# Kernel optimization log

Hardware: AMD Instinct MI355X
Metric: run time of the kernel (lower is better)

## Reference

```python
import jax, jax.numpy as jnp
import numpy as np

VOCAB, D, H, HK, DH, M, DFF, NCLS = 32000, 512, 8, 2, 64, 64, 2048, 2
G = H // HK  # GQA group size = 4
EPS = 1e-6


def rmsnorm(x, g):
    return x * jax.lax.rsqrt(jnp.mean(x * x, axis=-1, keepdims=True) + EPS) * g


def setup_inputs() -> dict:
    key = jax.random.key(0)
    ks = jax.random.split(key, 14)
    s = 0.02
    return {
        "input_ids": jax.random.randint(ks[0], (8, 8192), 0, VOCAB),
        "emb": jax.random.normal(ks[1], (VOCAB, D), jnp.float32) * s,
        "Wq": jax.random.normal(ks[2], (D, H * DH), jnp.float32) * s,
        "Wk": jax.random.normal(ks[3], (D, HK * DH), jnp.float32) * s,
        "Wv": jax.random.normal(ks[4], (D, HK * DH), jnp.float32) * s,
        "Wphi": jax.random.normal(ks[5], (DH, M), jnp.float32),  # Laplacian kernel feature projection
        "Wo": jax.random.normal(ks[6], (H * DH, D), jnp.float32) * s,
        "g1": jnp.ones((D,), jnp.float32),
        "g2": jnp.ones((D,), jnp.float32),
        "Wg": jax.random.normal(ks[7], (D, DFF), jnp.float32) * s,
        "Wu": jax.random.normal(ks[8], (D, DFF), jnp.float32) * s,  # frozen up_proj (freeze only affects training, not math)
        "Wd": jax.random.normal(ks[9], (DFF, D), jnp.float32) * s,
        "Wc": jax.random.normal(ks[10], (D, NCLS), jnp.float32) * s,
        "bc": jnp.zeros((NCLS,), jnp.float32),
    }


def reference(input_ids, emb, Wq, Wk, Wv, Wphi, Wo, g1, g2, Wg, Wu, Wd, Wc, bc):
    B, S = input_ids.shape
    x = emb[input_ids]  # [B,S,D] embedding gather
    # --- kernelized (Laplacian) bidirectional GQA linear attention, pre-norm ---
    h = rmsnorm(x, g1)
    q = (h @ Wq).reshape(B, S, H, DH)
    k = (h @ Wk).reshape(B, S, HK, DH)
    v = (h @ Wv).reshape(B, S, HK, DH)
    # Laplacian positive feature map: phi(u) = exp(-|u @ Wphi|)  -> [.., M]
    pq = jnp.exp(-jnp.abs(jnp.einsum("bshd,dm->bshm", q, Wphi)))
    pk = jnp.exp(-jnp.abs(jnp.einsum("bskd,dm->bskm", k, Wphi)))
    # global (bidirectional) state per kv head: [B,HK,M,DH] and normalizer [B,HK,M]
    kv = jnp.einsum("bskm,bskd->bkmd", pk, v)
    z = pk.sum(axis=1)
    pqg = pq.reshape(B, S, HK, G, M)  # group query heads onto kv heads
    num = jnp.einsum("bskgm,bkmd->bskgd", pqg, kv)
    den = jnp.einsum("bskgm,bkm->bskg", pqg, z)
    attn = (num / (den[..., None] + EPS)).reshape(B, S, H * DH)
    x = x + attn @ Wo
    # --- SwiGLU FFN, pre-norm ---
    h2 = rmsnorm(x, g2)
    x = x + (jax.nn.silu(h2 @ Wg) * (h2 @ Wu)) @ Wd
    # --- mean pool + linear head ---
    logits = x.mean(axis=1) @ Wc + bc  # [B, NCLS]
    return logits
```

## Files before the change

kernel.cpp:

```cpp
#include <hip/hip_runtime.h>
#include <hip/hip_bf16.h>
#include <math.h>

typedef __attribute__((ext_vector_type(8))) short bf16x8;
typedef __attribute__((ext_vector_type(4))) float f32x4;

#define DEV static __device__ __forceinline__
#define AS1 __attribute__((address_space(1)))
#define AS3 __attribute__((address_space(3)))

DEV float bf2f(__hip_bfloat16 v) { return __bfloat162float(v); }
DEV __hip_bfloat16 f2bf(float f) { return __float2bfloat16(f); }
DEV float us2f(unsigned short u) { return __uint_as_float(((unsigned int)u) << 16); }
DEV unsigned short f2us(float f) {
    __hip_bfloat16 b = __float2bfloat16(f);
    return *(unsigned short*)&b;
}

DEV void gload_lds16(const void* g, void* l) {
    __builtin_amdgcn_global_load_lds((const AS1 unsigned int*)g,
                                     (AS3 unsigned int*)l, 16, 0, 0);
}

DEV void load8(const void* p, size_t off, int f32m, float* o) {
    if (f32m) {
        const float4* r = (const float4*)((const float*)p + off);
        float4 A = r[0], B = r[1];
        o[0] = A.x; o[1] = A.y; o[2] = A.z; o[3] = A.w;
        o[4] = B.x; o[5] = B.y; o[6] = B.z; o[7] = B.w;
    } else {
        const ushort4* r = (const ushort4*)((const __hip_bfloat16*)p + off);
        ushort4 A = r[0], B = r[1];
        o[0] = us2f(A.x); o[1] = us2f(A.y); o[2] = us2f(A.z); o[3] = us2f(A.w);
        o[4] = us2f(B.x); o[5] = us2f(B.y); o[6] = us2f(B.z); o[7] = us2f(B.w);
    }
}

DEV float loadElem(const void* p, size_t idx, int f32m) {
    return f32m ? ((const float*)p)[idx] : bf2f(((const __hip_bfloat16*)p)[idx]);
}

constexpr int NTOK = 65536;

constexpr size_t OFF_WQPT = 0;
constexpr size_t OFF_WKPT = OFF_WQPT + 524288ull;
constexpr size_t OFF_WVT  = OFF_WKPT + 131072ull;
constexpr size_t OFF_WOT  = OFF_WVT  + 131072ull;
constexpr size_t OFF_WGT  = OFF_WOT  + 524288ull;
constexpr size_t OFF_WUT  = OFF_WGT  + 2097152ull;
constexpr size_t OFF_KV   = OFF_WUT  + 2097152ull;
constexpr size_t OFF_Z    = OFF_KV   + 262144ull;
constexpr size_t OFF_POOL = OFF_Z    + 4096ull;
constexpr size_t OFF_TSUM = OFF_POOL + 16384ull;
constexpr size_t OFF_FLAG = OFF_TSUM + 65536ull;
constexpr size_t PERSIST  = OFF_FLAG + 256ull;
constexpr size_t OFF_H    = PERSIST;
constexpr size_t CHUNKBASE = OFF_H + 67108864ull;
constexpr int    ZERO_FLOATS = (262144 + 4096 + 16384 + 65536) / 4;
constexpr size_t PERTOK = 3584ull;

__global__ __launch_bounds__(128) void detect_kernel(
    const unsigned int* __restrict__ w, int* __restrict__ flag)
{
    __shared__ int cnt;
    if (threadIdx.x == 0) cnt = 0;
    __syncthreads();
    unsigned int v = w[threadIdx.x];
    float a = fabsf(us2f((unsigned short)(v & 0xFFFFu)));
    if (a >= 0.0625f && a <= 8.0f) atomicAdd(&cnt, 1);
    __syncthreads();
    if (threadIdx.x == 0) *flag = (cnt < 64) ? 1 : 0;
}

__global__ __launch_bounds__(256) void zero_kernel(float* __restrict__ p, int n)
{
    int i = blockIdx.x * 256 + threadIdx.x;
    if (i < n) p[i] = 0.0f;
}

__global__ __launch_bounds__(256) void fuse_phi_kernel(
    const void* __restrict__ W, const void* __restrict__ Wphi,
    __hip_bfloat16* __restrict__ outT, int wld, const int* __restrict__ flag)
{
    const int f = *flag;
    int o = blockIdx.x * 256 + threadIdx.x;
    int hm = o >> 9, d = o & 511;
    int h = hm >> 6, m = hm & 63;
    float acc = 0.f;
    if (f) {
        const float* Wf = (const float*)W;
        const float* Pf = (const float*)Wphi;
        #pragma unroll 8
        for (int dh = 0; dh < 64; ++dh)
            acc += Wf[(size_t)d * wld + h * 64 + dh] * Pf[dh * 64 + m];
    } else {
        const __hip_bfloat16* Wb = (const __hip_bfloat16*)W;
        const __hip_bfloat16* Pb = (const __hip_bfloat16*)Wphi;
        #pragma unroll 8
        for (int dh = 0; dh < 64; ++dh)
            acc += bf2f(Wb[(size_t)d * wld + h * 64 + dh]) * bf2f(Pb[dh * 64 + m]);
    }
    outT[o] = f2bf(acc);
}

__global__ __launch_bounds__(256) void transpose_kernel(
    const void* __restrict__ src, __hip_bfloat16* __restrict__ dst, int R, int Ccols,
    const int* __restrict__ flag)
{
    __shared__ float tile[32][33];
    const int f = *flag;
    const int tx = threadIdx.x & 31, ty = threadIdx.x >> 5;
    const int c0 = blockIdx.x * 32, r0 = blockIdx.y * 32;
    #pragma unroll
    for (int k = 0; k < 4; ++k) {
        const int rl = ty + k * 8;
        tile[rl][tx] = loadElem(src, (size_t)(r0 + rl) * Ccols + c0 + tx, f);
    }
    __syncthreads();
    #pragma unroll
    for (int k = 0; k < 4; ++k) {
        const int cl = ty + k * 8;
        dst[(size_t)(c0 + cl) * R + r0 + tx] = f2bf(tile[tx][cl]);
    }
}

__global__ __launch_bounds__(256) void embed_rms_kernel(
    const int* __restrict__ ids, const void* __restrict__ emb,
    const void* __restrict__ g1, __hip_bfloat16* __restrict__ h,
    const int* __restrict__ flag)
{
    const int f = *flag;
    const int n = blockIdx.x * 4 + (threadIdx.x >> 6);
    const int lane = threadIdx.x & 63;
    const int id = ids[n];
    float x[8];
    load8(emb, (size_t)id * 512 + lane * 8, f, x);
    float ss = 0.f;
    #pragma unroll
    for (int i = 0; i < 8; ++i) ss += x[i] * x[i];
    #pragma unroll
    for (int off = 32; off; off >>= 1) ss += __shfl_xor(ss, off, 64);
    const float scale = rsqrtf(ss * (1.0f / 512.0f) + 1e-6f);
    float gv[8];
    load8(g1, (size_t)lane * 8, f, gv);
    ushort4 h0, h1;
    h0.x = f2us(x[0] * scale * gv[0]); h0.y = f2us(x[1] * scale * gv[1]);
    h0.z = f2us(x[2] * scale * gv[2]); h0.w = f2us(x[3] * scale * gv[3]);
    h1.x = f2us(x[4] * scale * gv[4]); h1.y = f2us(x[5] * scale * gv[5]);
    h1.z = f2us(x[6] * scale * gv[6]); h1.w = f2us(x[7] * scale * gv[7]);
    ushort4* ho = (ushort4*)(h + (size_t)n * 512 + lane * 8);
    ho[0] = h0; ho[1] = h1;
}

__global__ __launch_bounds__(256) void rms2_kernel(
    const float* __restrict__ xf, const void* __restrict__ g2,
    __hip_bfloat16* __restrict__ h, const int* __restrict__ flag)
{
    const int f = *flag;
    const int n = blockIdx.x * 4 + (threadIdx.x >> 6);
    const int lane = threadIdx.x & 63;
    const float4* xr = (const float4*)(xf + (size_t)n * 512);
    float4 a = xr[lane * 2], b = xr[lane * 2 + 1];
    float x[8] = { a.x, a.y, a.z, a.w, b.x, b.y, b.z, b.w };
    float ss = 0.f;
    #pragma unroll
    for (int i = 0; i < 8; ++i) ss += x[i] * x[i];
    #pragma unroll
    for (int off = 32; off; off >>= 1) ss += __shfl_xor(ss, off, 64);
    const float scale = rsqrtf(ss * (1.0f / 512.0f) + 1e-6f);
    float gv[8];
    load8(g2, (size_t)lane * 8, f, gv);
    ushort4 h0, h1;
    h0.x = f2us(x[0] * scale * gv[0]); h0.y = f2us(x[1] * scale * gv[1]);
    h0.z = f2us(x[2] * scale * gv[2]); h0.w = f2us(x[3] * scale * gv[3]);
    h1.x = f2us(x[4] * scale * gv[4]); h1.y = f2us(x[5] * scale * gv[5]);
    h1.z = f2us(x[6] * scale * gv[6]); h1.w = f2us(x[7] * scale * gv[7]);
    ushort4* ho = (ushort4*)(h + (size_t)n * 512 + lane * 8);
    ho[0] = h0; ho[1] = h1;
}

template<int MODE>
__global__ __launch_bounds__(256) void gemm128_kernel(
    const __hip_bfloat16* __restrict__ A, const __hip_bfloat16* __restrict__ Bt,
    float* __restrict__ xf, __hip_bfloat16* __restrict__ Cout2,
    float* __restrict__ pooled, const int* __restrict__ ids,
    const void* __restrict__ emb, const int* __restrict__ flag, int gbase, int K)
{
    __shared__ __align__(16) char As[8192];
    __shared__ __align__(16) char Bs[8192];
    __shared__ int idsL[128];

    const int tid = threadIdx.x;
    const int bm = blockIdx.x, bn = blockIdx.y;
    const int wave = tid >> 6, lane = tid & 63;
    const int quad = lane >> 4, lr = lane & 15;
    const int wm = (wave >> 1) << 6, wn = (wave & 1) << 6;

    if (MODE == 7 && tid < 128) idsL[tid] = ids[bm * 128 + tid];

    const int srow = (wave << 5) + (lane >> 2);
    const int scol = lane & 3;
    const int sfr  = (srow + (srow >> 2)) & 3;
    const int sofs = ((scol ^ sfr) << 3);

    const __hip_bfloat16* ga0 = A  + (size_t)(bm * 128 + srow) * K + sofs;
    const __hip_bfloat16* gb0 = Bt + (size_t)(bn * 128 + srow) * K + sofs;
    const __hip_bfloat16* ga1 = ga0 + (size_t)16 * K;
    const __hip_bfloat16* gb1 = gb0 + (size_t)16 * K;
    char* lA0 = As + (wave << 11);
    char* lA1 = lA0 + 1024;
    char* lB0 = Bs + (wave << 11);
    char* lB1 = lB0 + 1024;

    const int fl  = (lr + (lr >> 2)) & 3;
    const int ac  = (quad ^ fl) << 4;
    const char* arp = As + ((wm + lr) << 6) + ac;
    const char* brp = Bs + ((wn + lr) << 6) + ac;

    f32x4 acc[4][4];
    #pragma unroll
    for (int i = 0; i < 4; ++i)
        #pragma unroll
        for (int j = 0; j < 4; ++j)
            #pragma unroll
            for (int r = 0; r < 4; ++r) acc[i][j][r] = 0.0f;

    for (int k0 = 0; k0 < K; k0 += 32) {
        __syncthreads();
        gload_lds16(ga0 + k0, lA0);
        gload_lds16(ga1 + k0, lA1);
        gload_lds16(gb0 + k0, lB0);
        gload_lds16(gb1 + k0, lB1);
        __syncthreads();

        bf16x8 af[4], bfr[4];
        #pragma unroll
        for (int i = 0; i < 4; ++i)
            af[i] = *(const bf16x8*)(arp + i * 1024);
        #pragma unroll
        for (int j = 0; j < 4; ++j)
            bfr[j] = *(const bf16x8*)(brp + j * 1024);
        #pragma unroll
        for (int i = 0; i < 4; ++i)
            #pragma unroll
            for (int j = 0; j < 4; ++j)
                acc[i][j] = __builtin_amdgcn_mfma_f32_16x16x32_bf16(af[i], bfr[j], acc[i][j], 0, 0, 0);
    }

    const int col0 = bn * 128 + wn + lr;

    if (MODE == 7) {
        const int f = *flag;
        const int b = (gbase + bm * 128) >> 13;
        #pragma unroll
        for (int j = 0; j < 4; ++j) {
            const int col = col0 + j * 16;
            float s = 0.f;
            #pragma unroll
            for (int i = 0; i < 4; ++i)
                #pragma unroll
                for (int r = 0; r < 4; ++r) {
                    const int rl = wm + i * 16 + quad * 4 + r;
                    const float e = loadElem(emb, (size_t)idsL[rl] * 512 + col, f);
                    const float w = e + acc[i][j][r];
                    xf[(size_t)(bm * 128 + rl) * 512 + col] = w;
                    s += w;
                }
            s += __shfl_xor(s, 16, 64);
            s += __shfl_xor(s, 32, 64);
            if (quad == 0) atomicAdd(&pooled[b * 512 + col], s);
        }
        return;
    }

    const int row0 = bm * 128 + wm + quad * 4;
    #pragma unroll
    for (int i = 0; i < 4; ++i)
        #pragma unroll
        for (int j = 0; j < 4; ++j) {
            const int col = col0 + j * 16;
            #pragma unroll
            for (int r = 0; r < 4; ++r) {
                const int row = row0 + i * 16 + r;
                const float v = acc[i][j][r];
                Cout2[(size_t)row * 256 + col] = f2bf(bn == 0 ? expf(-fabsf(v)) : v);
            }
        }
}

__global__ __launch_bounds__(256, 2) void pq_mix_kernel(
    const __hip_bfloat16* __restrict__ h, const __hip_bfloat16* __restrict__ WQPt,
    const float* __restrict__ kvf, const float* __restrict__ zf,
    __hip_bfloat16* __restrict__ attn, int gbase, int K)
{
    __shared__ __align__(16) char As[8192];
    __shared__ __align__(16) char Bs[8192];
    __shared__ __align__(16) char Pl[128 * 272];
    __shared__ __align__(16) __hip_bfloat16 kvT[80][72];

    const int tid = threadIdx.x;
    const int bm = blockIdx.x, bn = blockIdx.y;
    const int kh = bn >> 1;
    const int wave = tid >> 6, lane = tid & 63;
    const int quad = lane >> 4, lr = lane & 15;
    const int wm = (wave >> 1) << 6, wn = (wave & 1) << 6;
    const int b = (gbase + bm * 128) >> 13;

    {
        const float* kvsrc = kvf + ((size_t)b * 2 + kh) * 4096;
        for (int i = tid; i < 4096; i += 256) {
            const int m = i >> 6, dh = i & 63;
            kvT[dh][m] = f2bf(kvsrc[i]);
        }
        if (tid < 64) kvT[64][tid] = f2bf(zf[((size_t)b * 2 + kh) * 64 + tid]);
        for (int i = tid; i < 15 * 64; i += 256)
            kvT[65 + (i >> 6)][i & 63] = f2bf(0.0f);
    }

    const int srow = (wave << 5) + (lane >> 2);
    const int scol = lane & 3;
    const int sfr  = (srow + (srow >> 2)) & 3;
    const int sofs = ((scol ^ sfr) << 3);

    const __hip_bfloat16* ga0 = h    + (size_t)(bm * 128 + srow) * K + sofs;
    const __hip_bfloat16* gb0 = WQPt + (size_t)(bn * 128 + srow) * K + sofs;
    const __hip_bfloat16* ga1 = ga0 + (size_t)16 * K;
    const __hip_bfloat16* gb1 = gb0 + (size_t)16 * K;
    char* lA0 = As + (wave << 11);
    char* lA1 = lA0 + 1024;
    char* lB0 = Bs + (wave << 11);
    char* lB1 = lB0 + 1024;

    const int fl  = (lr + (lr >> 2)) & 3;
    const int ac  = (quad ^ fl) << 4;
    const char* arp = As + ((wm + lr) << 6) + ac;
    const char* brp = Bs + ((wn + lr) << 6) + ac;

    f32x4 acc[4][4];
    #pragma unroll
    for (int i = 0; i < 4; ++i)
        #pragma unroll
        for (int j = 0; j < 4; ++j)
            #pragma unroll
            for (int r = 0; r < 4; ++r) acc[i][j][r] = 0.0f;

    for (int k0 = 0; k0 < K; k0 += 32) {
        __syncthreads();
        gload_lds16(ga0 + k0, lA0);
        gload_lds16(ga1 + k0, lA1);
        gload_lds16(gb0 + k0, lB0);
        gload_lds16(gb1 + k0, lB1);
        __syncthreads();

        bf16x8 af[4], bfr[4];
        #pragma unroll
        for (int i = 0; i < 4; ++i)
            af[i] = *(const bf16x8*)(arp + i * 1024);
        #pragma unroll
        for (int j = 0; j < 4; ++j)
            bfr[j] = *(const bf16x8*)(brp + j * 1024);
        #pragma unroll
        for (int i = 0; i < 4; ++i)
            #pragma unroll
            for (int j = 0; j < 4; ++j)
                acc[i][j] = __builtin_amdgcn_mfma_f32_16x16x32_bf16(af[i], bfr[j], acc[i][j], 0, 0, 0);
    }

    #pragma unroll
    for (int i = 0; i < 4; ++i)
        #pragma unroll
        for (int j = 0; j < 4; ++j)
            #pragma unroll
            for (int r = 0; r < 4; ++r) {
                const int rl = wm + i * 16 + quad * 4 + r;
                const int cl = wn + j * 16 + lr;
                *(__hip_bfloat16*)(Pl + rl * 272 + cl * 2) = f2bf(expf(-fabsf(acc[i][j][r])));
            }
    __syncthreads();

    const int hl = wave & 1;
    f32x4 acc2[4][5];
    #pragma unroll
    for (int i = 0; i < 4; ++i)
        #pragma unroll
        for (int j = 0; j < 5; ++j)
            #pragma unroll
            for (int r = 0; r < 4; ++r) acc2[i][j][r] = 0.0f;

    #pragma unroll
    for (int kk = 0; kk < 2; ++kk) {
        const int kofs = kk * 32 + quad * 8;
        bf16x8 af[4], bfr[5];
        #pragma unroll
        for (int i = 0; i < 4; ++i)
            af[i] = *(const bf16x8*)(Pl + (wm + i * 16 + lr) * 272 + (wn + kofs) * 2);
        #pragma unroll
        for (int j = 0; j < 5; ++j)
            bfr[j] = *(const bf16x8*)&kvT[j * 16 + lr][kofs];
        #pragma unroll
        for (int i = 0; i < 4; ++i)
            #pragma unroll
            for (int j = 0; j < 5; ++j)
                acc2[i][j] = __builtin_amdgcn_mfma_f32_16x16x32_bf16(af[i], bfr[j], acc2[i][j], 0, 0, 0);
    }

    const int colb = (bn * 2 + hl) * 64;
    #pragma unroll
    for (int i = 0; i < 4; ++i) {
        const int rowb = bm * 128 + wm + i * 16 + quad * 4;
        #pragma unroll
        for (int r = 0; r < 4; ++r) {
            const float den = __shfl(acc2[i][4][r], lane & 48, 64);
            const float inv = 1.0f / (den + 1e-6f);
            const size_t base = (size_t)(rowb + r) * 512 + colb;
            #pragma unroll
            for (int j = 0; j < 4; ++j)
                attn[base + j * 16 + lr] = f2bf(acc2[i][j][r] * inv);
        }
    }
}

__global__ __launch_bounds__(512, 2) void ffn8_kernel(
    const __hip_bfloat16* __restrict__ A, const __hip_bfloat16* __restrict__ Bg,
    const __hip_bfloat16* __restrict__ Bu, float* __restrict__ tsum, int gbase)
{
    __shared__ __align__(16) char L[131072];

    const int tid = threadIdx.x;
    const int bm = blockIdx.x;
    const int wave = tid >> 6, lane = tid & 63;
    const int quad = lane >> 4, lr = lane & 15;

    {
        const int ss = (lane & 56) | ((lane ^ wave) & 7);
        const __hip_bfloat16* gsrc = A + (size_t)(bm * 128 + wave) * 512 + ss * 8;
        char* ldst = L + wave * 1024;
        #pragma unroll
        for (int i = 0; i < 16; ++i)
            gload_lds16(gsrc + (size_t)i * 8 * 512, ldst + i * 8192);
    }
    asm volatile("s_waitcnt vmcnt(0)" ::: "memory");
    __syncthreads();

    const int x7s = (lr & 7) << 4;
    const char* apq = L + (lr << 10);

    const __hip_bfloat16* pG = Bg + (size_t)(wave * 256 + lr) * 512 + quad * 8;
    const __hip_bfloat16* pU = Bu + (size_t)(wave * 256 + lr) * 512 + quad * 8;

    const int b = (gbase + bm * 128) >> 13;

    for (int ci = 0; ci < 8; ++ci) {
        const __hip_bfloat16* pGc = pG + (size_t)ci * 32 * 512;
        const __hip_bfloat16* pUc = pU + (size_t)ci * 32 * 512;

        f32x4 aG[8][2], aU[8][2];
        #pragma unroll
        for (int m = 0; m < 8; ++m)
            #pragma unroll
            for (int c = 0; c < 2; ++c)
                #pragma unroll
                for (int r = 0; r < 4; ++r) { aG[m][c][r] = 0.0f; aU[m][c][r] = 0.0f; }

        #pragma unroll 2
        for (int ks = 0; ks < 16; ++ks) {
            const int so = ((ks << 6) | (quad << 4)) ^ x7s;
            bf16x8 af[8];
            #pragma unroll
            for (int m = 0; m < 8; ++m)
                af[m] = *(const bf16x8*)(apq + m * 16384 + so);
            bf16x8 bg0 = *(const bf16x8*)(pGc + ks * 32);
            bf16x8 bg1 = *(const bf16x8*)(pGc + 16 * 512 + ks * 32);
            bf16x8 bu0 = *(const bf16x8*)(pUc + ks * 32);
            bf16x8 bu1 = *(const bf16x8*)(pUc + 16 * 512 + ks * 32);
            #pragma unroll
            for (int m = 0; m < 8; ++m) {
                aG[m][0] = __builtin_amdgcn_mfma_f32_16x16x32_bf16(af[m], bg0, aG[m][0], 0, 0, 0);
                aG[m][1] = __builtin_amdgcn_mfma_f32_16x16x32_bf16(af[m], bg1, aG[m][1], 0, 0, 0);
                aU[m][0] = __builtin_amdgcn_mfma_f32_16x16x32_bf16(af[m], bu0, aU[m][0], 0, 0, 0);
                aU[m][1] = __builtin_amdgcn_mfma_f32_16x16x32_bf16(af[m], bu1, aU[m][1], 0, 0, 0);
            }
        }

        #pragma unroll
        for (int c = 0; c < 2; ++c) {
            float s = 0.f;
            #pragma unroll
            for (int m = 0; m < 8; ++m)
                #pragma unroll
                for (int r = 0; r < 4; ++r) {
                    const float g = aG[m][c][r];
                    s += (g / (1.0f + expf(-g))) * aU[m][c][r];
                }
            s += __shfl_xor(s, 16, 64);
            s += __shfl_xor(s, 32, 64);
            if (quad == 0)
                atomicAdd(&tsum[b * 2048 + wave * 256 + ci * 32 + c * 16 + lr], s);
        }
    }
}

__global__ __launch_bounds__(256) void ffn_pool_kernel(
    const float* __restrict__ tsum, const void* __restrict__ Wd,
    float* __restrict__ pooled, const int* __restrict__ flag)
{
    __shared__ float ts[8][64];
    const int f = *flag;
    const int k0 = blockIdx.x * 64;
    const int t = threadIdx.x;
    for (int i = t; i < 512; i += 256)
        ts[i >> 6][i & 63] = tsum[(i >> 6) * 2048 + k0 + (i & 63)];
    __syncthreads();

    float acc0[8] = {}, acc1[8] = {};
    for (int kk = 0; kk < 64; ++kk) {
        const size_t krow = (size_t)(k0 + kk) * 512;
        const float w0 = loadElem(Wd, krow + t, f);
        const float w1 = loadElem(Wd, krow + t + 256, f);
        #pragma unroll
        for (int b = 0; b < 8; ++b) {
            acc0[b] += ts[b][kk] * w0;
            acc1[b] += ts[b][kk] * w1;
        }
    }
    #pragma unroll
    for (int b = 0; b < 8; ++b) {
        atomicAdd(&pooled[b * 512 + t], acc0[b]);
        atomicAdd(&pooled[b * 512 + t + 256], acc1[b]);
    }
}

__global__ __launch_bounds__(256) void kv_z_kernel(
    const __hip_bfloat16* __restrict__ pkv,
    float* __restrict__ kv, float* __restrict__ z, int gbase, int nrows)
{
    __shared__ float pks[8][64], vs[8][64];
    const int slab = blockIdx.x, kh = blockIdx.y;
    const int b = (gbase + slab * nrows) >> 13;
    const int tid = threadIdx.x;
    const int tm = (tid & 15) << 2, tdh = (tid >> 4) << 2;
    const int lss = tid >> 5, lmm = (tid & 31) << 1;

    float acc[4][4] = {};
    float zacc[4] = {};
    for (int sb = 0; sb < nrows; sb += 8) {
        __syncthreads();
        {
            const size_t n = (size_t)slab * nrows + sb + lss;
            const __hip_bfloat16* pr = pkv + n * 256 + kh * 64 + lmm;
            const __hip_bfloat16* vr = pkv + n * 256 + 128 + kh * 64 + lmm;
            pks[lss][lmm]     = bf2f(pr[0]);
            pks[lss][lmm + 1] = bf2f(pr[1]);
            vs[lss][lmm]      = bf2f(vr[0]);
            vs[lss][lmm + 1]  = bf2f(vr[1]);
        }
        __syncthreads();
        #pragma unroll
        for (int ss = 0; ss < 8; ++ss) {
            f32x4 p = *(const f32x4*)&pks[ss][tm];
            f32x4 w = *(const f32x4*)&vs[ss][tdh];
            #pragma unroll
            for (int i = 0; i < 4; ++i)
                #pragma unroll
                for (int j = 0; j < 4; ++j)
                    acc[i][j] += p[i] * w[j];
            if ((tid >> 4) == 0) {
                #pragma unroll
                for (int i = 0; i < 4; ++i) zacc[i] += p[i];
            }
        }
    }
    #pragma unroll
    for (int i = 0; i < 4; ++i)
        #pragma unroll
        for (int j = 0; j < 4; ++j)
            atomicAdd(&kv[(((size_t)b * 2 + kh) * 64 + tm + i) * 64 + tdh + j], acc[i][j]);
    if ((tid >> 4) == 0) {
        #pragma unroll
        for (int i = 0; i < 4; ++i)
            atomicAdd(&z[((size_t)b * 2 + kh) * 64 + tm + i], zacc[i]);
    }
}

__global__ __launch_bounds__(256) void head_kernel(
    const float* __restrict__ pooled, const void* __restrict__ Wc,
    const void* __restrict__ bc, void* __restrict__ out, const int* __restrict__ flag)
{
    const int f = *flag;
    const int t = threadIdx.x;
    const int grp = t >> 4, ln = t & 15;
    const int b = grp >> 1, c = grp & 1;
    float p = 0.f;
    for (int d = ln; d < 512; d += 16)
        p += pooled[b * 512 + d] * loadElem(Wc, (size_t)d * 2 + c, f);
    #pragma unroll
    for (int off = 8; off; off >>= 1) p += __shfl_xor(p, off, 64);
    if (ln == 0) {
        const float val = p * (1.0f / 8192.0f) + loadElem(bc, c, f);
        if (f) ((float*)out)[b * 2 + c] = val;
        else   ((__hip_bfloat16*)out)[b * 2 + c] = f2bf(val);
    }
}

extern "C" void kernel_launch(void* const* d_in, const int* in_sizes, int n_in,
                              void* d_out, int out_size, void* d_ws, size_t ws_size,
                              hipStream_t stream)
{
    const int* ids   = (const int*)d_in[0];
    const void* emb  = d_in[1];
    const void* Wq   = d_in[2];
    const void* Wk   = d_in[3];
    const void* Wv   = d_in[4];
    const void* Wph  = d_in[5];
    const void* Wo   = d_in[6];
    const void* g1   = d_in[7];
    const void* g2   = d_in[8];
    const void* Wg   = d_in[9];
    const void* Wu   = d_in[10];
    const void* Wd   = d_in[11];
    const void* Wc   = d_in[12];
    const void* bc   = d_in[13];

    char* ws = (char*)d_ws;
    __hip_bfloat16* WQPt  = (__hip_bfloat16*)(ws + OFF_WQPT);
    __hip_bfloat16* WKPt  = (__hip_bfloat16*)(ws + OFF_WKPT);
    __hip_bfloat16* WvT   = (__hip_bfloat16*)(ws + OFF_WVT);
    __hip_bfloat16* WoT   = (__hip_bfloat16*)(ws + OFF_WOT);
    __hip_bfloat16* WgT   = (__hip_bfloat16*)(ws + OFF_WGT);
    __hip_bfloat16* WuT   = (__hip_bfloat16*)(ws + OFF_WUT);
    float*          kv    = (float*)(ws + OFF_KV);
    float*          z     = (float*)(ws + OFF_Z);
    float*          pooled= (float*)(ws + OFF_POOL);
    float*          tsum  = (float*)(ws + OFF_TSUM);
    int*            flag  = (int*)(ws + OFF_FLAG);
    __hip_bfloat16* hall  = (__hip_bfloat16*)(ws + OFF_H);

    int C = 65536;
    while (C > 256 && CHUNKBASE + PERTOK * (size_t)C > ws_size) C >>= 1;
    const int NC = NTOK / C;

    char* cb = ws + CHUNKBASE;
    float*          xf   = (float*)cb;
    __hip_bfloat16* attn = (__hip_bfloat16*)(cb + (size_t)C * 2048);
    __hip_bfloat16* pkv  = (__hip_bfloat16*)(cb + (size_t)C * 3072);

    detect_kernel<<<1, 128, 0, stream>>>((const unsigned int*)Wph, flag);
    zero_kernel<<<(ZERO_FLOATS + 255) / 256, 256, 0, stream>>>(kv, ZERO_FLOATS);

    fuse_phi_kernel<<<1024, 256, 0, stream>>>(Wq, Wph, WQPt, 512, flag);
    fuse_phi_kernel<<<256, 256, 0, stream>>>(Wk, Wph, WKPt, 128, flag);
    transpose_kernel<<<dim3(128 / 32, 512 / 32), 256, 0, stream>>>(Wv, WvT, 512, 128, flag);
    transpose_kernel<<<dim3(512 / 32, 512 / 32), 256, 0, stream>>>(Wo, WoT, 512, 512, flag);
    transpose_kernel<<<dim3(2048 / 32, 512 / 32), 256, 0, stream>>>(Wg, WgT, 512, 2048, flag);
    transpose_kernel<<<dim3(2048 / 32, 512 / 32), 256, 0, stream>>>(Wu, WuT, 512, 2048, flag);

    for (int c = 0; c < NC; ++c) {
        const int g0 = c * C;
        __hip_bfloat16* hc = hall + (size_t)g0 * 512;
        embed_rms_kernel<<<C / 4, 256, 0, stream>>>(ids + g0, emb, g1, hc, flag);
        gemm128_kernel<8><<<dim3(C / 128, 2), 256, 0, stream>>>(
            hc, WKPt, nullptr, pkv, nullptr, nullptr, nullptr, flag, g0, 512);
        kv_z_kernel<<<dim3(C / 128, 2), 256, 0, stream>>>(pkv, kv, z, g0, 128);
    }

    for (int c = 0; c < NC; ++c) {
        const int g0 = c * C;
        __hip_bfloat16* hc = hall + (size_t)g0 * 512;
        pq_mix_kernel<<<dim3(C / 128, 4), 256, 0, stream>>>(
            hc, WQPt, kv, z, attn, g0, 512);
        gemm128_kernel<7><<<dim3(C / 128, 4), 256, 0, stream>>>(
            attn, WoT, xf, nullptr, pooled, ids + g0, emb, flag, g0, 512);
        rms2_kernel<<<C / 4, 256, 0, stream>>>(xf, g2, hc, flag);
        ffn8_kernel<<<C / 128, 512, 0, stream>>>(hc, WgT, WuT, tsum, g0);
    }

    ffn_pool_kernel<<<32, 256, 0, stream>>>(tsum, Wd, pooled, flag);

    head_kernel<<<1, 256, 0, stream>>>(pooled, Wc, bc, d_out, flag);
}
```

Before: 909.4 us.

## Fuse Wo projection, residual, pooling and RMSNorm into the FFN kernel

The Wo GEMM, the embedding residual add, the mean-pool atomics and the second RMSNorm now run inside the FFN kernel's prologue on a 128-row tile held in LDS, replacing the separate gemm128<7> and rms2 kernels. This removes the fp32 xf round trip through global memory and the bf16 h rewrite, and it shrinks the per-token workspace so larger chunks fit. In exchange, each block recomputes the full 512-column Wo output with a large accumulator array, which raises register pressure and reduces parallelism for that stage. Wo weights are also read straight from global memory by every block.

```diff
diff --git a/kernel.cpp b/kernel.cpp
--- a/kernel.cpp
+++ b/kernel.cpp
@@ -57,7 +57,7 @@
 constexpr size_t OFF_H    = PERSIST;
 constexpr size_t CHUNKBASE = OFF_H + 67108864ull;
 constexpr int    ZERO_FLOATS = (262144 + 4096 + 16384 + 65536) / 4;
-constexpr size_t PERTOK = 3584ull;
+constexpr size_t PERTOK = 1536ull;
 
 __global__ __launch_bounds__(128) void detect_kernel(
     const unsigned int* __restrict__ w, int* __restrict__ flag)
@@ -152,51 +152,19 @@
     ho[0] = h0; ho[1] = h1;
 }
 
-__global__ __launch_bounds__(256) void rms2_kernel(
-    const float* __restrict__ xf, const void* __restrict__ g2,
-    __hip_bfloat16* __restrict__ h, const int* __restrict__ flag)
-{
-    const int f = *flag;
-    const int n = blockIdx.x * 4 + (threadIdx.x >> 6);
-    const int lane = threadIdx.x & 63;
-    const float4* xr = (const float4*)(xf + (size_t)n * 512);
-    float4 a = xr[lane * 2], b = xr[lane * 2 + 1];
-    float x[8] = { a.x, a.y, a.z, a.w, b.x, b.y, b.z, b.w };
-    float ss = 0.f;
-    #pragma unroll
-    for (int i = 0; i < 8; ++i) ss += x[i] * x[i];
-    #pragma unroll
-    for (int off = 32; off; off >>= 1) ss += __shfl_xor(ss, off, 64);
-    const float scale = rsqrtf(ss * (1.0f / 512.0f) + 1e-6f);
-    float gv[8];
-    load8(g2, (size_t)lane * 8, f, gv);
-    ushort4 h0, h1;
-    h0.x = f2us(x[0] * scale * gv[0]); h0.y = f2us(x[1] * scale * gv[1]);
-    h0.z = f2us(x[2] * scale * gv[2]); h0.w = f2us(x[3] * scale * gv[3]);
-    h1.x = f2us(x[4] * scale * gv[4]); h1.y = f2us(x[5] * scale * gv[5]);
-    h1.z = f2us(x[6] * scale * gv[6]); h1.w = f2us(x[7] * scale * gv[7]);
-    ushort4* ho = (ushort4*)(h + (size_t)n * 512 + lane * 8);
-    ho[0] = h0; ho[1] = h1;
-}
-
 template<int MODE>
 __global__ __launch_bounds__(256) void gemm128_kernel(
     const __hip_bfloat16* __restrict__ A, const __hip_bfloat16* __restrict__ Bt,
-    float* __restrict__ xf, __hip_bfloat16* __restrict__ Cout2,
-    float* __restrict__ pooled, const int* __restrict__ ids,
-    const void* __restrict__ emb, const int* __restrict__ flag, int gbase, int K)
+    __hip_bfloat16* __restrict__ Cout2, const int* __restrict__ flag, int gbase, int K)
 {
     __shared__ __align__(16) char As[8192];
     __shared__ __align__(16) char Bs[8192];
-    __shared__ int idsL[128];
 
     const int tid = threadIdx.x;
     const int bm = blockIdx.x, bn = blockIdx.y;
     const int wave = tid >> 6, lane = tid & 63;
     const int quad = lane >> 4, lr = lane & 15;
     const int wm = (wave >> 1) << 6, wn = (wave & 1) << 6;
-
-    if (MODE == 7 && tid < 128) idsL[tid] = ids[bm * 128 + tid];
 
     const int srow = (wave << 5) + (lane >> 2);
     const int scol = lane & 3;
@@ -249,30 +217,6 @@
 
     const int col0 = bn * 128 + wn + lr;
 
-    if (MODE == 7) {
-        const int f = *flag;
-        const int b = (gbase + bm * 128) >> 13;
-        #pragma unroll
-        for (int j = 0; j < 4; ++j) {
-            const int col = col0 + j * 16;
-            float s = 0.f;
-            #pragma unroll
-            for (int i = 0; i < 4; ++i)
-                #pragma unroll
-                for (int r = 0; r < 4; ++r) {
-                    const int rl = wm + i * 16 + quad * 4 + r;
-                    const float e = loadElem(emb, (size_t)idsL[rl] * 512 + col, f);
-                    const float w = e + acc[i][j][r];
-                    xf[(size_t)(bm * 128 + rl) * 512 + col] = w;
-                    s += w;
-                }
-            s += __shfl_xor(s, 16, 64);
-            s += __shfl_xor(s, 32, 64);
-            if (quad == 0) atomicAdd(&pooled[b * 512 + col], s);
-        }
-        return;
-    }
-
     const int row0 = bm * 128 + wm + quad * 4;
     #pragma unroll
     for (int i = 0; i < 4; ++i)
@@ -420,20 +364,30 @@
     }
 }
 
-__global__ __launch_bounds__(512, 2) void ffn8_kernel(
-    const __hip_bfloat16* __restrict__ A, const __hip_bfloat16* __restrict__ Bg,
-    const __hip_bfloat16* __restrict__ Bu, float* __restrict__ tsum, int gbase)
+__global__ __launch_bounds__(512, 2) void wo_ffn_kernel(
+    const __hip_bfloat16* __restrict__ attn, const __hip_bfloat16* __restrict__ WoT,
+    const __hip_bfloat16* __restrict__ Bg, const __hip_bfloat16* __restrict__ Bu,
+    const int* __restrict__ ids, const void* __restrict__ emb, const void* __restrict__ g2,
+    float* __restrict__ pooled, float* __restrict__ tsum,
+    const int* __restrict__ flag, int gbase)
 {
     __shared__ __align__(16) char L[131072];
+    __shared__ int   idsL[128];
+    __shared__ float rssW[8][128];
+    __shared__ float scaleL[128];
 
     const int tid = threadIdx.x;
     const int bm = blockIdx.x;
     const int wave = tid >> 6, lane = tid & 63;
     const int quad = lane >> 4, lr = lane & 15;
+    const int f = *flag;
+    const int b = (gbase + bm * 128) >> 13;
+
+    if (tid < 128) idsL[tid] = ids[bm * 128 + tid];
 
     {
         const int ss = (lane & 56) | ((lane ^ wave) & 7);
-        const __hip_bfloat16* gsrc = A + (size_t)(bm * 128 + wave) * 512 + ss * 8;
+        const __hip_bfloat16* gsrc = attn + (size_t)(bm * 128 + wave) * 512 + ss * 8;
         char* ldst = L + wave * 1024;
         #pragma unroll
         for (int i = 0; i < 16; ++i)
@@ -445,10 +399,95 @@
     const int x7s = (lr & 7) << 4;
     const char* apq = L + (lr << 10);
 
+    {
+        const __hip_bfloat16* pW = WoT + (size_t)(wave * 64 + lr) * 512 + quad * 8;
+        f32x4 acc[8][4];
+        #pragma unroll
+        for (int m = 0; m < 8; ++m)
+            #pragma unroll
+            for (int c = 0; c < 4; ++c)
+                #pragma unroll
+                for (int r = 0; r < 4; ++r) acc[m][c][r] = 0.0f;
+
+        #pragma unroll 2
+        for (int ks = 0; ks < 16; ++ks) {
+            const int so = ((ks << 6) | (quad << 4)) ^ x7s;
+            bf16x8 af[8];
+            #pragma unroll
+            for (int m = 0; m < 8; ++m)
+                af[m] = *(const bf16x8*)(apq + m * 16384 + so);
+            bf16x8 bw[4];
+            #pragma unroll
+            for (int c = 0; c < 4; ++c)
+                bw[c] = *(const bf16x8*)(pW + (size_t)c * 16 * 512 + ks * 32);
+            #pragma unroll
+            for (int m = 0; m < 8; ++m)
+                #pragma unroll
+                for (int c = 0; c < 4; ++c)
+                    acc[m][c] = __builtin_amdgcn_mfma_f32_16x16x32_bf16(af[m], bw[c], acc[m][c], 0, 0, 0);
+        }
+        __syncthreads();
+
+        #pragma unroll
+        for (int c = 0; c < 4; ++c) {
+            const int col = wave * 64 + c * 16 + lr;
+            float s = 0.f;
+            #pragma unroll
+            for (int m = 0; m < 8; ++m)
+                #pragma unroll
+                for (int r = 0; r < 4; ++r) {
+                    const int row = m * 16 + quad * 4 + r;
+                    const float e = loadElem(emb, (size_t)idsL[row] * 512 + col, f);
+                    acc[m][c][r] += e;
+                    s += acc[m][c][r];
+                }
+            s += __shfl_xor(s, 16, 64);
+            s += __shfl_xor(s, 32, 64);
+            if (quad == 0) atomicAdd(&pooled[b * 512 + col], s);
+        }
+        #pragma unroll
+        for (int m = 0; m < 8; ++m)
+            #pragma unroll
+            for (int r = 0; r < 4; ++r) {
+                float q = 0.f;
+                #pragma unroll
+                for (int c = 0; c < 4; ++c) q += acc[m][c][r] * acc[m][c][r];
+                q += __shfl_xor(q, 1, 64);
+                q += __shfl_xor(q, 2, 64);
+                q += __shfl_xor(q, 4, 64);
+                q += __shfl_xor(q, 8, 64);
+                if (lr == 0) rssW[wave][m * 16 + quad * 4 + r] = q;
+            }
+        __syncthreads();
+        if (tid < 128) {
+            float t = 0.f;
+            #pragma unroll
+            for (int w = 0; w < 8; ++w) t += rssW[w][tid];
+            scaleL[tid] = rsqrtf(t * (1.0f / 512.0f) + 1e-6f);
+        }
+        __syncthreads();
+
+        float g2v[4];
+        #pragma unroll
+        for (int c = 0; c < 4; ++c) g2v[c] = loadElem(g2, wave * 64 + c * 16 + lr, f);
+        #pragma unroll
+        for (int m = 0; m < 8; ++m)
+            #pragma unroll
+            for (int r = 0; r < 4; ++r) {
+                const int row = m * 16 + quad * 4 + r;
+                const float sc = scaleL[row];
+                #pragma unroll
+                for (int c = 0; c < 4; ++c) {
+                    const int col = wave * 64 + c * 16 + lr;
+                    const int byte_ = row * 1024 + (((col >> 3) ^ (row & 7)) << 4) + (col & 7) * 2;
+                    *(unsigned short*)(L + byte_) = f2us(acc[m][c][r] * sc * g2v[c]);
+                }
+            }
+    }
+    __syncthreads();
+
     const __hip_bfloat16* pG = Bg + (size_t)(wave * 256 + lr) * 512 + quad * 8;
     const __hip_bfloat16* pU = Bu + (size_t)(wave * 256 + lr) * 512 + quad * 8;
-
-    const int b = (gbase + bm * 128) >> 13;
 
     for (int ci = 0; ci < 8; ++ci) {
         const __hip_bfloat16* pGc = pG + (size_t)ci * 32 * 512;
@@ -640,9 +679,8 @@
     const int NC = NTOK / C;
 
     char* cb = ws + CHUNKBASE;
-    float*          xf   = (float*)cb;
-    __hip_bfloat16* attn = (__hip_bfloat16*)(cb + (size_t)C * 2048);
-    __hip_bfloat16* pkv  = (__hip_bfloat16*)(cb + (size_t)C * 3072);
+    __hip_bfloat16* attn = (__hip_bfloat16*)cb;
+    __hip_bfloat16* pkv  = (__hip_bfloat16*)(cb + (size_t)C * 1024);
 
     detect_kernel<<<1, 128, 0, stream>>>((const unsigned int*)Wph, flag);
     zero_kernel<<<(ZERO_FLOATS + 255) / 256, 256, 0, stream>>>(kv, ZERO_FLOATS);
@@ -659,7 +697,7 @@
         __hip_bfloat16* hc = hall + (size_t)g0 * 512;
         embed_rms_kernel<<<C / 4, 256, 0, stream>>>(ids + g0, emb, g1, hc, flag);
         gemm128_kernel<8><<<dim3(C / 128, 2), 256, 0, stream>>>(
-            hc, WKPt, nullptr, pkv, nullptr, nullptr, nullptr, flag, g0, 512);
+            hc, WKPt, pkv, flag, g0, 512);
         kv_z_kernel<<<dim3(C / 128, 2), 256, 0, stream>>>(pkv, kv, z, g0, 128);
     }
 
@@ -668,10 +706,8 @@
         __hip_bfloat16* hc = hall + (size_t)g0 * 512;
         pq_mix_kernel<<<dim3(C / 128, 4), 256, 0, stream>>>(
             hc, WQPt, kv, z, attn, g0, 512);
-        gemm128_kernel<7><<<dim3(C / 128, 4), 256, 0, stream>>>(
-            attn, WoT, xf, nullptr, pooled, ids + g0, emb, flag, g0, 512);
-        rms2_kernel<<<C / 4, 256, 0, stream>>>(xf, g2, hc, flag);
-        ffn8_kernel<<<C / 128, 512, 0, stream>>>(hc, WgT, WuT, tsum, g0);
+        wo_ffn_kernel<<<C / 128, 512, 0, stream>>>(
+            attn, WoT, WgT, WuT, ids + g0, emb, g2, pooled, tsum, flag, g0);
     }
 
     ffn_pool_kernel<<<32, 256, 0, stream>>>(tsum, Wd, pooled, flag);
```

Measured after the change: 810.7 us (median of 2 runs). -10.9%, faster.
